# Optimization experiments

Measured on AMD Instinct MI355X. Metric: run time of the kernel, lower is better.

## Reference

```python
import math
import jax, jax.numpy as jnp
import numpy as np

B, T, C, H = 2, 2048, 1024, 16

def setup_inputs() -> dict:
    key = jax.random.key(0)
    k1, k2, k3 = jax.random.split(key, 3)
    x = jax.random.normal(k1, (B, T, C), dtype=jnp.float32)
    W_kqv = jax.random.normal(k2, (C, 3 * C), dtype=jnp.float32) * (1.0 / math.sqrt(C))
    W_proj = jax.random.normal(k3, (C, C), dtype=jnp.float32) * (1.0 / math.sqrt(C))
    b_proj = jnp.zeros((C,), dtype=jnp.float32)
    return {"x": x, "W_kqv": W_kqv, "W_proj": W_proj, "b_proj": b_proj}

def reference(x, W_kqv, W_proj, b_proj):
    Bx, Tx, Cx = x.shape
    hs = Cx // H  # head size
    q, k, v = jnp.split(x @ W_kqv, 3, axis=2)  # each (B,T,C)
    # (B,T,C) -> (B,H,T,hs)
    q = q.reshape(Bx, Tx, H, hs).transpose(0, 2, 1, 3)
    k = k.reshape(Bx, Tx, H, hs).transpose(0, 2, 1, 3)
    v = v.reshape(Bx, Tx, H, hs).transpose(0, 2, 1, 3)
    attn = jnp.einsum('bhqd,bhkd->bhqk', q, k) / math.sqrt(hs)  # (B,H,T,T)
    causal = jnp.tril(jnp.ones((Tx, Tx), dtype=bool))
    attn = jnp.where(causal, attn, -jnp.inf)
    attn = jax.nn.softmax(attn, axis=-1)
    y = jnp.einsum('bhqk,bhkd->bhqd', attn, v)  # (B,H,T,hs)
    y = y.transpose(0, 2, 1, 3).reshape(Bx, Tx, Cx)
    return y @ W_proj + b_proj
```

## Files before the change

### kernel.cpp

```cpp
#include <hip/hip_runtime.h>


typedef unsigned short u16;
typedef unsigned int u32;
typedef __bf16 bf16x8 __attribute__((ext_vector_type(8)));
typedef float f32x4 __attribute__((ext_vector_type(4)));
typedef u32 u32x4 __attribute__((ext_vector_type(4)));
typedef u16 u16x4 __attribute__((ext_vector_type(4)));

__device__ __forceinline__ u16 f2bf(float f) {
  u32 u = __float_as_uint(f);
  u32 r = u + 0x7FFFu + ((u >> 16) & 1u);
  return (u16)(r >> 16);
}

__device__ __forceinline__ bf16x8 ld_bf8(const u16* p) {
  union { u32x4 u; bf16x8 b; } x;
  x.u = *(const u32x4*)p;
  return x.b;
}

__device__ __forceinline__ void gld_lds16(const u16* g, u16* l) {
  __builtin_amdgcn_global_load_lds(
      (const __attribute__((address_space(1))) u32*)g,
      (__attribute__((address_space(3))) u32*)l, 16, 0, 0);
}

__global__ __launch_bounds__(256) void conv_x_kernel(const float* __restrict__ src,
                                                     u16* __restrict__ dst) {
  int idx = blockIdx.x * 256 + threadIdx.x;
  const float4* s4 = (const float4*)src;
  float4 a = s4[2 * idx], b = s4[2 * idx + 1];
  union { u16 h[8]; u32x4 v; } pk;
  pk.h[0] = f2bf(a.x); pk.h[1] = f2bf(a.y); pk.h[2] = f2bf(a.z); pk.h[3] = f2bf(a.w);
  pk.h[4] = f2bf(b.x); pk.h[5] = f2bf(b.y); pk.h[6] = f2bf(b.z); pk.h[7] = f2bf(b.w);
  *(u32x4*)&dst[(size_t)idx * 8] = pk.v;
}

__global__ __launch_bounds__(256) void convT_kernel(const float* __restrict__ src,
                                                    u16* __restrict__ dst, int R, int Cc) {
  __shared__ float ls[64][65];
  int r0 = blockIdx.x * 64, c0 = blockIdx.y * 64;
  int t = threadIdx.x;
  for (int u = t; u < 1024; u += 256) {
    int r = u >> 4, cs = (u & 15) << 2;
    float4 v = *(const float4*)&src[(size_t)(r0 + r) * Cc + (c0 + cs)];
    ls[r][cs] = v.x; ls[r][cs + 1] = v.y; ls[r][cs + 2] = v.z; ls[r][cs + 3] = v.w;
  }
  __syncthreads();
  for (int u = t; u < 1024; u += 256) {
    int n = u >> 4, ks = (u & 15) << 2;
    u16x4 o;
    o.x = f2bf(ls[ks][n]); o.y = f2bf(ls[ks + 1][n]);
    o.z = f2bf(ls[ks + 2][n]); o.w = f2bf(ls[ks + 3][n]);
    *(u16x4*)&dst[(size_t)(c0 + n) * R + (r0 + ks)] = o;
  }
}

__global__ __launch_bounds__(512) void qkv_gemm_kernel(
    const u16* __restrict__ A, const u16* __restrict__ Bt,
    u16* __restrict__ Qh, u16* __restrict__ Kh, u16* __restrict__ Vh, float qscale) {
  constexpr int K = 1024;
  __shared__ __align__(16) u16 As[128 * 32];
  __shared__ __align__(16) u16 Bs[128 * 32];
  int t = threadIdx.x;
  int wave = t >> 6, lane = t & 63, quad = lane >> 4, l16 = lane & 15;
  int wm = (wave >> 1) << 5, wn = (wave & 1) << 6;
  int m0 = blockIdx.x * 128, n0 = blockIdx.y * 128;
  f32x4 acc[2][4] = {};
  int u0 = t;
  int ra0 = u0 >> 2, ca0 = ((u0 & 3) ^ ((u0 >> 3) & 3)) << 3;
  int swq = (quad ^ ((l16 >> 1) & 3)) << 3;
  for (int k0 = 0; k0 < K; k0 += 32) {
    gld_lds16(&A[(size_t)(m0 + ra0) * K + k0 + ca0], &As[u0 * 8]);
    gld_lds16(&Bt[(size_t)(n0 + ra0) * K + k0 + ca0], &Bs[u0 * 8]);
    __syncthreads();
    bf16x8 af[2], bfr[4];
    for (int r = 0; r < 2; ++r) af[r] = ld_bf8(&As[(wm + r * 16 + l16) * 32 + swq]);
    for (int c = 0; c < 4; ++c) bfr[c] = ld_bf8(&Bs[(wn + c * 16 + l16) * 32 + swq]);
    for (int r = 0; r < 2; ++r)
      for (int c = 0; c < 4; ++c)
        acc[r][c] = __builtin_amdgcn_mfma_f32_16x16x32_bf16(af[r], bfr[c], acc[r][c], 0, 0, 0);
    __syncthreads();
  }
  for (int r = 0; r < 2; ++r) {
    int rowbase = m0 + wm + r * 16 + quad * 4;
    for (int c = 0; c < 4; ++c) {
      int col = n0 + wn + c * 16 + l16;
      int seg = col >> 10;
      int cc = col & 1023;
      int h = cc >> 6, d = cc & 63;
      for (int i = 0; i < 4; ++i) {
        int row = rowbase + i;
        int b = row >> 11, tt = row & 2047;
        size_t off = (((size_t)(b * 16 + h)) * 2048 + tt) * 64 + d;
        float v = acc[r][c][i];
        if (seg == 0)      Qh[off] = f2bf(v * qscale);
        else if (seg == 1) Kh[off] = f2bf(v);
        else               Vh[off] = f2bf(v);
      }
    }
  }
}

__global__ __launch_bounds__(256) void vT_kernel(const u16* __restrict__ Vh,
                                                 u16* __restrict__ Vt) {
  __shared__ __align__(16) u16 ls[64 * 72];
  int t = threadIdx.x;
  int t0 = blockIdx.x * 64, bh = blockIdx.y;
  const u16* in = Vh + ((size_t)bh * 2048 + t0) * 64;
  for (int u = t; u < 512; u += 256) {
    int row = u >> 3, col = (u & 7) << 3;
    *(u32x4*)&ls[row * 72 + col] = *(const u32x4*)&in[(size_t)row * 64 + col];
  }
  __syncthreads();
  for (int u = t; u < 512; u += 256) {
    int d = u >> 3, tc = (u & 7) << 3;
    union { u16 h[8]; u32x4 v; } pk;
    for (int j = 0; j < 8; ++j) pk.h[j] = ls[(tc + j) * 72 + d];
    *(u32x4*)&Vt[((size_t)bh * 64 + d) * 2048 + t0 + tc] = pk.v;
  }
}

__global__ __launch_bounds__(256) void proj_gemm_kernel(
    const u16* __restrict__ A, const u16* __restrict__ Bt,
    float* __restrict__ out, const float* __restrict__ bias) {
  constexpr int K = 1024;
  __shared__ __align__(16) u16 As[64 * 32];
  __shared__ __align__(16) u16 Bs[64 * 32];
  int t = threadIdx.x;
  int wave = t >> 6, lane = t & 63, quad = lane >> 4, l16 = lane & 15;
  int wm = (wave >> 1) << 5, wn = (wave & 1) << 5;
  int m0 = blockIdx.x * 64, n0 = blockIdx.y * 64;
  f32x4 acc[2][2] = {};
  int u0 = t;
  int ra0 = u0 >> 2, ca0 = ((u0 & 3) ^ ((u0 >> 3) & 3)) << 3;
  int swq = (quad ^ ((l16 >> 1) & 3)) << 3;
  for (int k0 = 0; k0 < K; k0 += 32) {
    gld_lds16(&A[(size_t)(m0 + ra0) * K + k0 + ca0], &As[u0 * 8]);
    gld_lds16(&Bt[(size_t)(n0 + ra0) * K + k0 + ca0], &Bs[u0 * 8]);
    __syncthreads();
    bf16x8 af[2], bfr[2];
    for (int r = 0; r < 2; ++r) af[r] = ld_bf8(&As[(wm + r * 16 + l16) * 32 + swq]);
    for (int c = 0; c < 2; ++c) bfr[c] = ld_bf8(&Bs[(wn + c * 16 + l16) * 32 + swq]);
    for (int r = 0; r < 2; ++r)
      for (int c = 0; c < 2; ++c)
        acc[r][c] = __builtin_amdgcn_mfma_f32_16x16x32_bf16(af[r], bfr[c], acc[r][c], 0, 0, 0);
    __syncthreads();
  }
  for (int r = 0; r < 2; ++r) {
    int rowbase = m0 + wm + r * 16 + quad * 4;
    for (int c = 0; c < 2; ++c) {
      int col = n0 + wn + c * 16 + l16;
      float bv = bias[col];
      for (int i = 0; i < 4; ++i)
        out[(size_t)(rowbase + i) * 1024 + col] = acc[r][c][i] + bv;
    }
  }
}

__global__ __launch_bounds__(256) void flash_kernel(
    const u16* __restrict__ Qh, const u16* __restrict__ Kh, const u16* __restrict__ Vt,
    u16* __restrict__ yb) {
  constexpr int LDK = 72;
  __shared__ __align__(16) u16 Ks[64 * LDK];
  __shared__ __align__(16) u16 Vs[64 * LDK];
  __shared__ __align__(16) u16 Ps[64 * LDK];
  int t = threadIdx.x, wave = t >> 6, lane = t & 63, quad = lane >> 4, l16 = lane & 15;
  int qtile = 31 - blockIdx.x;
  int bh = blockIdx.y;
  int q0 = qtile << 6;
  const u16* Qb = Qh + (size_t)bh * 2048 * 64;
  const u16* Kb = Kh + (size_t)bh * 2048 * 64;
  const u16* Vb = Vt + (size_t)bh * 64 * 2048;
  bf16x8 qa0, qa1;
  {
    int qrow = q0 + wave * 16 + l16;
    qa0 = ld_bf8(&Qb[(size_t)qrow * 64 + quad * 8]);
    qa1 = ld_bf8(&Qb[(size_t)qrow * 64 + 32 + quad * 8]);
  }
  bf16x8 onesf;
  {
    union { u16 h[8]; bf16x8 b; } o;
    u16 v = (l16 == 0) ? (u16)0x3F80 : (u16)0;
    for (int i = 0; i < 8; ++i) o.h[i] = v;
    onesf = o.b;
  }
  f32x4 oacc[4] = {};
  f32x4 lacc = {};
  int nkv = qtile + 1;
  int r1 = t >> 3, s1 = (t & 7) << 3, r2 = r1 + 32;
  u32x4 kreg0, kreg1, vreg0, vreg1;
  kreg0 = *(const u32x4*)&Kb[(size_t)r1 * 64 + s1];
  kreg1 = *(const u32x4*)&Kb[(size_t)r2 * 64 + s1];
  vreg0 = *(const u32x4*)&Vb[(size_t)r1 * 2048 + s1];
  vreg1 = *(const u32x4*)&Vb[(size_t)r2 * 2048 + s1];
  for (int j = 0; j < nkv; ++j) {
    __syncthreads();
    *(u32x4*)&Ks[r1 * LDK + s1] = kreg0;
    *(u32x4*)&Ks[r2 * LDK + s1] = kreg1;
    *(u32x4*)&Vs[r1 * LDK + s1] = vreg0;
    *(u32x4*)&Vs[r2 * LDK + s1] = vreg1;
    __syncthreads();
    if (j + 1 < nkv) {
      int kv0 = (j + 1) << 6;
      kreg0 = *(const u32x4*)&Kb[(size_t)(kv0 + r1) * 64 + s1];
      kreg1 = *(const u32x4*)&Kb[(size_t)(kv0 + r2) * 64 + s1];
      vreg0 = *(const u32x4*)&Vb[(size_t)r1 * 2048 + kv0 + s1];
      vreg1 = *(const u32x4*)&Vb[(size_t)r2 * 2048 + kv0 + s1];
    }
    f32x4 s[4];
    for (int c = 0; c < 4; ++c) {
      bf16x8 kb0 = ld_bf8(&Ks[(c * 16 + l16) * LDK + quad * 8]);
      bf16x8 kb1 = ld_bf8(&Ks[(c * 16 + l16) * LDK + 32 + quad * 8]);
      f32x4 z = {0.f, 0.f, 0.f, 0.f};
      z = __builtin_amdgcn_mfma_f32_16x16x32_bf16(qa0, kb0, z, 0, 0, 0);
      s[c] = __builtin_amdgcn_mfma_f32_16x16x32_bf16(qa1, kb1, z, 0, 0, 0);
    }
    bool diag = (j == nkv - 1);
    for (int c = 0; c < 4; ++c)
      for (int i = 0; i < 4; ++i) {
        float p = __builtin_amdgcn_exp2f(s[c][i]);
        if (diag && (c * 16 + l16 > wave * 16 + quad * 4 + i)) p = 0.f;
        Ps[(wave * 16 + quad * 4 + i) * LDK + c * 16 + l16] = f2bf(p);
      }
    bf16x8 pa0 = ld_bf8(&Ps[(wave * 16 + l16) * LDK + quad * 8]);
    bf16x8 pa1 = ld_bf8(&Ps[(wave * 16 + l16) * LDK + 32 + quad * 8]);
    lacc = __builtin_amdgcn_mfma_f32_16x16x32_bf16(pa0, onesf, lacc, 0, 0, 0);
    lacc = __builtin_amdgcn_mfma_f32_16x16x32_bf16(pa1, onesf, lacc, 0, 0, 0);
    for (int dt = 0; dt < 4; ++dt) {
      bf16x8 vb0 = ld_bf8(&Vs[(dt * 16 + l16) * LDK + quad * 8]);
      bf16x8 vb1 = ld_bf8(&Vs[(dt * 16 + l16) * LDK + 32 + quad * 8]);
      oacc[dt] = __builtin_amdgcn_mfma_f32_16x16x32_bf16(pa0, vb0, oacc[dt], 0, 0, 0);
      oacc[dt] = __builtin_amdgcn_mfma_f32_16x16x32_bf16(pa1, vb1, oacc[dt], 0, 0, 0);
    }
  }
  int b = bh >> 4, h = bh & 15;
  for (int i = 0; i < 4; ++i) {
    float l = __shfl(lacc[i], quad * 16);
    float inv = 1.0f / l;
    int qq = q0 + wave * 16 + quad * 4 + i;
    size_t rowoff = ((size_t)(b * 2048 + qq)) * 1024 + h * 64;
    for (int dt = 0; dt < 4; ++dt)
      yb[rowoff + dt * 16 + l16] = f2bf(oacc[dt][i] * inv);
  }
}

extern "C" void kernel_launch(void* const* d_in, const int* in_sizes, int n_in,
                              void* d_out, int out_size, void* d_ws, size_t ws_size,
                              hipStream_t stream) {
  const float* x     = (const float*)d_in[0];
  const float* Wkqv  = (const float*)d_in[1];
  const float* Wproj = (const float*)d_in[2];
  const float* bproj = (const float*)d_in[3];
  float* out = (float*)d_out;

  u16* ws     = (u16*)d_ws;
  u16* xb     = ws;
  u16* wkqvT  = xb + (size_t)4096 * 1024;
  u16* wprojT = wkqvT + (size_t)3072 * 1024;
  u16* Qh     = wprojT + (size_t)1024 * 1024;
  u16* Kh     = Qh + (size_t)32 * 2048 * 64;
  u16* Vt     = Kh + (size_t)32 * 2048 * 64;
  u16* yb     = Vt + (size_t)32 * 2048 * 64;
  u16* Vh     = yb;

  const float QSCALE = 0.18033688011112042f;

  conv_x_kernel<<<2048, 256, 0, stream>>>(x, xb);
  convT_kernel<<<dim3(16, 48), 256, 0, stream>>>(Wkqv, wkqvT, 1024, 3072);
  convT_kernel<<<dim3(16, 16), 256, 0, stream>>>(Wproj, wprojT, 1024, 1024);
  qkv_gemm_kernel<<<dim3(32, 24), 512, 0, stream>>>(xb, wkqvT, Qh, Kh, Vh, QSCALE);
  vT_kernel<<<dim3(32, 32), 256, 0, stream>>>(Vh, Vt);
  flash_kernel<<<dim3(32, 32), 256, 0, stream>>>(Qh, Kh, Vt, yb);
  proj_gemm_kernel<<<dim3(64, 16), 256, 0, stream>>>(yb, wprojT, out, bproj);
}
```

Before: 203.7 us.

## Split long causal query tiles across two blocks and merge with a combine kernel

The 13 longest causal query tiles per head are each split into two halves of their KV range, run as separate blocks. Each half writes unnormalized fp32 partial outputs and row sums to scratch, and a new combine kernel adds the halves and normalizes. The aim is to even out the causal work imbalance across blocks. The QK MFMA operands are also swapped, so each lane holds a query row; the row sum is then taken in registers with two shuffles instead of an extra ones-MFMA, and P is stored to LDS as 4-wide vectors. The cost is an extra launch plus fp32 scratch traffic, with the scratch aliased over workspace regions that are no longer needed.

```diff
diff --git a/kernel.cpp b/kernel.cpp
--- a/kernel.cpp
+++ b/kernel.cpp
@@ -161,14 +161,23 @@
 
 __global__ __launch_bounds__(256) void flash_kernel(
     const u16* __restrict__ Qh, const u16* __restrict__ Kh, const u16* __restrict__ Vt,
-    u16* __restrict__ yb) {
+    u16* __restrict__ yb, float* __restrict__ Opart) {
   constexpr int LDK = 72;
   __shared__ __align__(16) u16 Ks[64 * LDK];
   __shared__ __align__(16) u16 Vs[64 * LDK];
   __shared__ __align__(16) u16 Ps[64 * LDK];
   int t = threadIdx.x, wave = t >> 6, lane = t & 63, quad = lane >> 4, l16 = lane & 15;
-  int qtile = 31 - blockIdx.x;
-  int bh = blockIdx.y;
+  int jx = blockIdx.x, bh = blockIdx.y;
+  int qtile, kvs, kve, sidx = 0, half = 0;
+  bool partial;
+  if (jx < 19) {
+    qtile = 18 - jx; kvs = 0; kve = qtile + 1; partial = false;
+  } else {
+    sidx = (jx - 19) >> 1; half = (jx - 19) & 1;
+    qtile = 31 - sidx;
+    int nkv = qtile + 1, mid = nkv >> 1;
+    kvs = half ? mid : 0; kve = half ? nkv : mid; partial = true;
+  }
   int q0 = qtile << 6;
   const u16* Qb = Qh + (size_t)bh * 2048 * 64;
   const u16* Kb = Kh + (size_t)bh * 2048 * 64;
@@ -179,55 +188,54 @@
     qa0 = ld_bf8(&Qb[(size_t)qrow * 64 + quad * 8]);
     qa1 = ld_bf8(&Qb[(size_t)qrow * 64 + 32 + quad * 8]);
   }
-  bf16x8 onesf;
-  {
-    union { u16 h[8]; bf16x8 b; } o;
-    u16 v = (l16 == 0) ? (u16)0x3F80 : (u16)0;
-    for (int i = 0; i < 8; ++i) o.h[i] = v;
-    onesf = o.b;
-  }
   f32x4 oacc[4] = {};
-  f32x4 lacc = {};
-  int nkv = qtile + 1;
+  float lsum = 0.f;
   int r1 = t >> 3, s1 = (t & 7) << 3, r2 = r1 + 32;
   u32x4 kreg0, kreg1, vreg0, vreg1;
-  kreg0 = *(const u32x4*)&Kb[(size_t)r1 * 64 + s1];
-  kreg1 = *(const u32x4*)&Kb[(size_t)r2 * 64 + s1];
-  vreg0 = *(const u32x4*)&Vb[(size_t)r1 * 2048 + s1];
-  vreg1 = *(const u32x4*)&Vb[(size_t)r2 * 2048 + s1];
-  for (int j = 0; j < nkv; ++j) {
+  {
+    int kv0 = kvs << 6;
+    kreg0 = *(const u32x4*)&Kb[(size_t)(kv0 + r1) * 64 + s1];
+    kreg1 = *(const u32x4*)&Kb[(size_t)(kv0 + r2) * 64 + s1];
+    vreg0 = *(const u32x4*)&Vb[(size_t)r1 * 2048 + kv0 + s1];
+    vreg1 = *(const u32x4*)&Vb[(size_t)r2 * 2048 + kv0 + s1];
+  }
+  for (int j = kvs; j < kve; ++j) {
+    int kv0 = j << 6;
     __syncthreads();
     *(u32x4*)&Ks[r1 * LDK + s1] = kreg0;
     *(u32x4*)&Ks[r2 * LDK + s1] = kreg1;
     *(u32x4*)&Vs[r1 * LDK + s1] = vreg0;
     *(u32x4*)&Vs[r2 * LDK + s1] = vreg1;
     __syncthreads();
-    if (j + 1 < nkv) {
-      int kv0 = (j + 1) << 6;
-      kreg0 = *(const u32x4*)&Kb[(size_t)(kv0 + r1) * 64 + s1];
-      kreg1 = *(const u32x4*)&Kb[(size_t)(kv0 + r2) * 64 + s1];
-      vreg0 = *(const u32x4*)&Vb[(size_t)r1 * 2048 + kv0 + s1];
-      vreg1 = *(const u32x4*)&Vb[(size_t)r2 * 2048 + kv0 + s1];
+    if (j + 1 < kve) {
+      int kn = (j + 1) << 6;
+      kreg0 = *(const u32x4*)&Kb[(size_t)(kn + r1) * 64 + s1];
+      kreg1 = *(const u32x4*)&Kb[(size_t)(kn + r2) * 64 + s1];
+      vreg0 = *(const u32x4*)&Vb[(size_t)r1 * 2048 + kn + s1];
+      vreg1 = *(const u32x4*)&Vb[(size_t)r2 * 2048 + kn + s1];
     }
     f32x4 s[4];
     for (int c = 0; c < 4; ++c) {
       bf16x8 kb0 = ld_bf8(&Ks[(c * 16 + l16) * LDK + quad * 8]);
       bf16x8 kb1 = ld_bf8(&Ks[(c * 16 + l16) * LDK + 32 + quad * 8]);
       f32x4 z = {0.f, 0.f, 0.f, 0.f};
-      z = __builtin_amdgcn_mfma_f32_16x16x32_bf16(qa0, kb0, z, 0, 0, 0);
-      s[c] = __builtin_amdgcn_mfma_f32_16x16x32_bf16(qa1, kb1, z, 0, 0, 0);
-    }
-    bool diag = (j == nkv - 1);
-    for (int c = 0; c < 4; ++c)
+      z = __builtin_amdgcn_mfma_f32_16x16x32_bf16(kb0, qa0, z, 0, 0, 0);
+      s[c] = __builtin_amdgcn_mfma_f32_16x16x32_bf16(kb1, qa1, s[c] = z, 0, 0, 0);
+    }
+    bool diag = (j == qtile);
+    int qg = q0 + wave * 16 + l16;
+    for (int c = 0; c < 4; ++c) {
+      union { u16 h[4]; u16x4 v; } pk;
       for (int i = 0; i < 4; ++i) {
         float p = __builtin_amdgcn_exp2f(s[c][i]);
-        if (diag && (c * 16 + l16 > wave * 16 + quad * 4 + i)) p = 0.f;
-        Ps[(wave * 16 + quad * 4 + i) * LDK + c * 16 + l16] = f2bf(p);
+        if (diag && (kv0 + c * 16 + quad * 4 + i > qg)) p = 0.f;
+        lsum += p;
+        pk.h[i] = f2bf(p);
       }
+      *(u16x4*)&Ps[(wave * 16 + l16) * LDK + c * 16 + quad * 4] = pk.v;
+    }
     bf16x8 pa0 = ld_bf8(&Ps[(wave * 16 + l16) * LDK + quad * 8]);
     bf16x8 pa1 = ld_bf8(&Ps[(wave * 16 + l16) * LDK + 32 + quad * 8]);
-    lacc = __builtin_amdgcn_mfma_f32_16x16x32_bf16(pa0, onesf, lacc, 0, 0, 0);
-    lacc = __builtin_amdgcn_mfma_f32_16x16x32_bf16(pa1, onesf, lacc, 0, 0, 0);
     for (int dt = 0; dt < 4; ++dt) {
       bf16x8 vb0 = ld_bf8(&Vs[(dt * 16 + l16) * LDK + quad * 8]);
       bf16x8 vb1 = ld_bf8(&Vs[(dt * 16 + l16) * LDK + 32 + quad * 8]);
@@ -235,15 +243,41 @@
       oacc[dt] = __builtin_amdgcn_mfma_f32_16x16x32_bf16(pa1, vb1, oacc[dt], 0, 0, 0);
     }
   }
+  lsum += __shfl_xor(lsum, 16);
+  lsum += __shfl_xor(lsum, 32);
+  if (partial) {
+    float* Op = Opart + ((size_t)(bh * 13 + sidx) * 2 + half) * 4160;
+    for (int dt = 0; dt < 4; ++dt)
+      for (int i = 0; i < 4; ++i)
+        Op[(wave * 16 + quad * 4 + i) * 64 + dt * 16 + l16] = oacc[dt][i];
+    if (quad == 0) Op[4096 + wave * 16 + l16] = lsum;
+  } else {
+    int b = bh >> 4, h = bh & 15;
+    for (int i = 0; i < 4; ++i) {
+      float inv = 1.0f / __shfl(lsum, quad * 4 + i);
+      int qq = q0 + wave * 16 + quad * 4 + i;
+      size_t rowoff = ((size_t)(b * 2048 + qq)) * 1024 + h * 64;
+      for (int dt = 0; dt < 4; ++dt)
+        yb[rowoff + dt * 16 + l16] = f2bf(oacc[dt][i] * inv);
+    }
+  }
+}
+
+__global__ __launch_bounds__(256) void combine_kernel(const float* __restrict__ Opart,
+                                                      u16* __restrict__ yb) {
+  int sidx = blockIdx.x, bh = blockIdx.y, t = threadIdx.x;
+  int qtile = 31 - sidx;
+  const float* A = Opart + (size_t)(bh * 13 + sidx) * 2 * 4160;
+  const float* Bp = A + 4160;
+  int q = t >> 2, d0 = (t & 3) << 4;
+  float inv = 1.0f / (A[4096 + q] + Bp[4096 + q]);
   int b = bh >> 4, h = bh & 15;
-  for (int i = 0; i < 4; ++i) {
-    float l = __shfl(lacc[i], quad * 16);
-    float inv = 1.0f / l;
-    int qq = q0 + wave * 16 + quad * 4 + i;
-    size_t rowoff = ((size_t)(b * 2048 + qq)) * 1024 + h * 64;
-    for (int dt = 0; dt < 4; ++dt)
-      yb[rowoff + dt * 16 + l16] = f2bf(oacc[dt][i] * inv);
-  }
+  size_t off = ((size_t)(b * 2048 + (qtile << 6) + q)) * 1024 + h * 64 + d0;
+  union { u16 h[16]; u32x4 v[2]; } pk;
+  for (int k = 0; k < 16; ++k)
+    pk.h[k] = f2bf((A[q * 64 + d0 + k] + Bp[q * 64 + d0 + k]) * inv);
+  *(u32x4*)&yb[off] = pk.v[0];
+  *(u32x4*)&yb[off + 8] = pk.v[1];
 }
 
 extern "C" void kernel_launch(void* const* d_in, const int* in_sizes, int n_in,
@@ -264,6 +298,7 @@
   u16* Vt     = Kh + (size_t)32 * 2048 * 64;
   u16* yb     = Vt + (size_t)32 * 2048 * 64;
   u16* Vh     = yb;
+  float* Opart = (float*)ws;
 
   const float QSCALE = 0.18033688011112042f;
 
@@ -272,6 +307,7 @@
   convT_kernel<<<dim3(16, 16), 256, 0, stream>>>(Wproj, wprojT, 1024, 1024);
   qkv_gemm_kernel<<<dim3(32, 24), 512, 0, stream>>>(xb, wkqvT, Qh, Kh, Vh, QSCALE);
   vT_kernel<<<dim3(32, 32), 256, 0, stream>>>(Vh, Vt);
-  flash_kernel<<<dim3(32, 32), 256, 0, stream>>>(Qh, Kh, Vt, yb);
+  flash_kernel<<<dim3(45, 32), 256, 0, stream>>>(Qh, Kh, Vt, yb, Opart);
+  combine_kernel<<<dim3(13, 32), 256, 0, stream>>>(Opart, yb);
   proj_gemm_kernel<<<dim3(64, 16), 256, 0, stream>>>(yb, wprojT, out, bproj);
 }
```

Result: faster. 191.4 us (-6.0%).

## Split long causal attention tiles across blocks and retile QKV and projection GEMMs

Applied to the files above, without the earlier changes.

The flash kernel moves to 128-row query tiles and maps 22 jobs per head through constant tables. The six longest query tiles are each split into two KV halves, which write fp32 partial outputs and row sums to workspace; a new combine kernel merges them, the aim being to balance causal work across blocks. Row sums are now taken with VALU adds and shuffles instead of an extra MFMA against a ones vector, and the K/V/P shared-memory layouts use an XOR-style swizzle in place of padding. Both GEMMs are retiled: QKV runs 4x4 MFMA tiles per wave with 256 threads, and projection uses 128x128 blocks with 512 threads. The costs are an extra launch, partial-result traffic through workspace that aliases the earlier buffers, and higher register pressure.

```diff
diff --git a/kernel.cpp b/kernel.cpp
--- a/kernel.cpp
+++ b/kernel.cpp
@@ -7,6 +7,9 @@
 typedef float f32x4 __attribute__((ext_vector_type(4)));
 typedef u32 u32x4 __attribute__((ext_vector_type(4)));
 typedef u16 u16x4 __attribute__((ext_vector_type(4)));
+
+__constant__ signed char JM[22] = {9,8,7,15,15,14,14,6,13,13,12,12,5,11,11,10,10,4,3,2,1,0};
+__constant__ signed char JH[22] = {0,0,0,1, 2, 1, 2, 0,1, 2, 1, 2, 0,1, 2, 1, 2, 0,0,0,0,0};
 
 __device__ __forceinline__ u16 f2bf(float f) {
   u32 u = __float_as_uint(f);
@@ -57,7 +60,7 @@
   }
 }
 
-__global__ __launch_bounds__(512) void qkv_gemm_kernel(
+__global__ __launch_bounds__(256) void qkv_gemm_kernel(
     const u16* __restrict__ A, const u16* __restrict__ Bt,
     u16* __restrict__ Qh, u16* __restrict__ Kh, u16* __restrict__ Vh, float qscale) {
   constexpr int K = 1024;
@@ -65,25 +68,28 @@
   __shared__ __align__(16) u16 Bs[128 * 32];
   int t = threadIdx.x;
   int wave = t >> 6, lane = t & 63, quad = lane >> 4, l16 = lane & 15;
-  int wm = (wave >> 1) << 5, wn = (wave & 1) << 6;
+  int wm = (wave >> 1) << 6, wn = (wave & 1) << 6;
   int m0 = blockIdx.x * 128, n0 = blockIdx.y * 128;
-  f32x4 acc[2][4] = {};
-  int u0 = t;
+  f32x4 acc[4][4] = {};
+  int u0 = t, u1 = t + 256;
   int ra0 = u0 >> 2, ca0 = ((u0 & 3) ^ ((u0 >> 3) & 3)) << 3;
+  int ra1 = u1 >> 2, ca1 = ((u1 & 3) ^ ((u1 >> 3) & 3)) << 3;
   int swq = (quad ^ ((l16 >> 1) & 3)) << 3;
   for (int k0 = 0; k0 < K; k0 += 32) {
     gld_lds16(&A[(size_t)(m0 + ra0) * K + k0 + ca0], &As[u0 * 8]);
+    gld_lds16(&A[(size_t)(m0 + ra1) * K + k0 + ca1], &As[u1 * 8]);
     gld_lds16(&Bt[(size_t)(n0 + ra0) * K + k0 + ca0], &Bs[u0 * 8]);
-    __syncthreads();
-    bf16x8 af[2], bfr[4];
-    for (int r = 0; r < 2; ++r) af[r] = ld_bf8(&As[(wm + r * 16 + l16) * 32 + swq]);
+    gld_lds16(&Bt[(size_t)(n0 + ra1) * K + k0 + ca1], &Bs[u1 * 8]);
+    __syncthreads();
+    bf16x8 af[4], bfr[4];
+    for (int r = 0; r < 4; ++r) af[r] = ld_bf8(&As[(wm + r * 16 + l16) * 32 + swq]);
     for (int c = 0; c < 4; ++c) bfr[c] = ld_bf8(&Bs[(wn + c * 16 + l16) * 32 + swq]);
-    for (int r = 0; r < 2; ++r)
+    for (int r = 0; r < 4; ++r)
       for (int c = 0; c < 4; ++c)
         acc[r][c] = __builtin_amdgcn_mfma_f32_16x16x32_bf16(af[r], bfr[c], acc[r][c], 0, 0, 0);
     __syncthreads();
   }
-  for (int r = 0; r < 2; ++r) {
+  for (int r = 0; r < 4; ++r) {
     int rowbase = m0 + wm + r * 16 + quad * 4;
     for (int c = 0; c < 4; ++c) {
       int col = n0 + wn + c * 16 + l16;
@@ -122,17 +128,17 @@
   }
 }
 
-__global__ __launch_bounds__(256) void proj_gemm_kernel(
+__global__ __launch_bounds__(512) void proj_gemm_kernel(
     const u16* __restrict__ A, const u16* __restrict__ Bt,
     float* __restrict__ out, const float* __restrict__ bias) {
   constexpr int K = 1024;
-  __shared__ __align__(16) u16 As[64 * 32];
-  __shared__ __align__(16) u16 Bs[64 * 32];
+  __shared__ __align__(16) u16 As[128 * 32];
+  __shared__ __align__(16) u16 Bs[128 * 32];
   int t = threadIdx.x;
   int wave = t >> 6, lane = t & 63, quad = lane >> 4, l16 = lane & 15;
-  int wm = (wave >> 1) << 5, wn = (wave & 1) << 5;
-  int m0 = blockIdx.x * 64, n0 = blockIdx.y * 64;
-  f32x4 acc[2][2] = {};
+  int wm = (wave >> 2) << 6, wn = (wave & 3) << 5;
+  int m0 = blockIdx.x * 128, n0 = blockIdx.y * 128;
+  f32x4 acc[4][2] = {};
   int u0 = t;
   int ra0 = u0 >> 2, ca0 = ((u0 & 3) ^ ((u0 >> 3) & 3)) << 3;
   int swq = (quad ^ ((l16 >> 1) & 3)) << 3;
@@ -140,15 +146,15 @@
     gld_lds16(&A[(size_t)(m0 + ra0) * K + k0 + ca0], &As[u0 * 8]);
     gld_lds16(&Bt[(size_t)(n0 + ra0) * K + k0 + ca0], &Bs[u0 * 8]);
     __syncthreads();
-    bf16x8 af[2], bfr[2];
-    for (int r = 0; r < 2; ++r) af[r] = ld_bf8(&As[(wm + r * 16 + l16) * 32 + swq]);
+    bf16x8 af[4], bfr[2];
+    for (int r = 0; r < 4; ++r) af[r] = ld_bf8(&As[(wm + r * 16 + l16) * 32 + swq]);
     for (int c = 0; c < 2; ++c) bfr[c] = ld_bf8(&Bs[(wn + c * 16 + l16) * 32 + swq]);
-    for (int r = 0; r < 2; ++r)
+    for (int r = 0; r < 4; ++r)
       for (int c = 0; c < 2; ++c)
         acc[r][c] = __builtin_amdgcn_mfma_f32_16x16x32_bf16(af[r], bfr[c], acc[r][c], 0, 0, 0);
     __syncthreads();
   }
-  for (int r = 0; r < 2; ++r) {
+  for (int r = 0; r < 4; ++r) {
     int rowbase = m0 + wm + r * 16 + quad * 4;
     for (int c = 0; c < 2; ++c) {
       int col = n0 + wn + c * 16 + l16;
@@ -161,88 +167,135 @@
 
 __global__ __launch_bounds__(256) void flash_kernel(
     const u16* __restrict__ Qh, const u16* __restrict__ Kh, const u16* __restrict__ Vt,
-    u16* __restrict__ yb) {
-  constexpr int LDK = 72;
-  __shared__ __align__(16) u16 Ks[64 * LDK];
-  __shared__ __align__(16) u16 Vs[64 * LDK];
-  __shared__ __align__(16) u16 Ps[64 * LDK];
+    u16* __restrict__ yb, float* __restrict__ Opart) {
+  __shared__ __align__(16) u16 Ks[64 * 64];
+  __shared__ __align__(16) u16 Vs[64 * 64];
+  __shared__ __align__(16) u16 Ps[128 * 64];
   int t = threadIdx.x, wave = t >> 6, lane = t & 63, quad = lane >> 4, l16 = lane & 15;
-  int qtile = 31 - blockIdx.x;
-  int bh = blockIdx.y;
-  int q0 = qtile << 6;
+  int jx = blockIdx.x, bh = blockIdx.y;
+  int m = JM[jx], jh = JH[jx];
+  int kvs = (jh == 2) ? (m + 1) : 0;
+  int kve = (jh == 1) ? (m + 1) : (2 * m + 2);
+  bool partial = jh != 0;
+  int q0 = m << 7;
   const u16* Qb = Qh + (size_t)bh * 2048 * 64;
   const u16* Kb = Kh + (size_t)bh * 2048 * 64;
   const u16* Vb = Vt + (size_t)bh * 64 * 2048;
-  bf16x8 qa0, qa1;
+  bf16x8 qa[2][2];
+  for (int s = 0; s < 2; ++s) {
+    int qrow = q0 + wave * 32 + s * 16 + l16;
+    qa[s][0] = ld_bf8(&Qb[(size_t)qrow * 64 + quad * 8]);
+    qa[s][1] = ld_bf8(&Qb[(size_t)qrow * 64 + 32 + quad * 8]);
+  }
+  f32x4 oacc[2][4] = {};
+  float ls0 = 0.f, ls1 = 0.f;
+  int ua = t, ub = t + 256;
+  int ra = ua >> 3, cba = ua & 7, rb = ub >> 3, cbb = ub & 7;
+  int lka = ra * 64 + ((cba + ra) & 7) * 8;
+  int lkb = rb * 64 + ((cbb + rb) & 7) * 8;
+  u32x4 kreg0, kreg1, vreg0, vreg1;
   {
-    int qrow = q0 + wave * 16 + l16;
-    qa0 = ld_bf8(&Qb[(size_t)qrow * 64 + quad * 8]);
-    qa1 = ld_bf8(&Qb[(size_t)qrow * 64 + 32 + quad * 8]);
-  }
-  bf16x8 onesf;
-  {
-    union { u16 h[8]; bf16x8 b; } o;
-    u16 v = (l16 == 0) ? (u16)0x3F80 : (u16)0;
-    for (int i = 0; i < 8; ++i) o.h[i] = v;
-    onesf = o.b;
-  }
-  f32x4 oacc[4] = {};
-  f32x4 lacc = {};
-  int nkv = qtile + 1;
-  int r1 = t >> 3, s1 = (t & 7) << 3, r2 = r1 + 32;
-  u32x4 kreg0, kreg1, vreg0, vreg1;
-  kreg0 = *(const u32x4*)&Kb[(size_t)r1 * 64 + s1];
-  kreg1 = *(const u32x4*)&Kb[(size_t)r2 * 64 + s1];
-  vreg0 = *(const u32x4*)&Vb[(size_t)r1 * 2048 + s1];
-  vreg1 = *(const u32x4*)&Vb[(size_t)r2 * 2048 + s1];
-  for (int j = 0; j < nkv; ++j) {
-    __syncthreads();
-    *(u32x4*)&Ks[r1 * LDK + s1] = kreg0;
-    *(u32x4*)&Ks[r2 * LDK + s1] = kreg1;
-    *(u32x4*)&Vs[r1 * LDK + s1] = vreg0;
-    *(u32x4*)&Vs[r2 * LDK + s1] = vreg1;
-    __syncthreads();
-    if (j + 1 < nkv) {
-      int kv0 = (j + 1) << 6;
-      kreg0 = *(const u32x4*)&Kb[(size_t)(kv0 + r1) * 64 + s1];
-      kreg1 = *(const u32x4*)&Kb[(size_t)(kv0 + r2) * 64 + s1];
-      vreg0 = *(const u32x4*)&Vb[(size_t)r1 * 2048 + kv0 + s1];
-      vreg1 = *(const u32x4*)&Vb[(size_t)r2 * 2048 + kv0 + s1];
-    }
-    f32x4 s[4];
+    int kv0 = kvs << 6;
+    kreg0 = *(const u32x4*)&Kb[(size_t)(kv0 + ra) * 64 + cba * 8];
+    kreg1 = *(const u32x4*)&Kb[(size_t)(kv0 + rb) * 64 + cbb * 8];
+    vreg0 = *(const u32x4*)&Vb[(size_t)ra * 2048 + kv0 + cba * 8];
+    vreg1 = *(const u32x4*)&Vb[(size_t)rb * 2048 + kv0 + cbb * 8];
+  }
+  for (int j = kvs; j < kve; ++j) {
+    int kv0 = j << 6;
+    __syncthreads();
+    *(u32x4*)&Ks[lka] = kreg0;
+    *(u32x4*)&Ks[lkb] = kreg1;
+    *(u32x4*)&Vs[lka] = vreg0;
+    *(u32x4*)&Vs[lkb] = vreg1;
+    __syncthreads();
+    if (j + 1 < kve) {
+      int kn = (j + 1) << 6;
+      kreg0 = *(const u32x4*)&Kb[(size_t)(kn + ra) * 64 + cba * 8];
+      kreg1 = *(const u32x4*)&Kb[(size_t)(kn + rb) * 64 + cbb * 8];
+      vreg0 = *(const u32x4*)&Vb[(size_t)ra * 2048 + kn + cba * 8];
+      vreg1 = *(const u32x4*)&Vb[(size_t)rb * 2048 + kn + cbb * 8];
+    }
+    bool maskit = (j >= 2 * m);
     for (int c = 0; c < 4; ++c) {
-      bf16x8 kb0 = ld_bf8(&Ks[(c * 16 + l16) * LDK + quad * 8]);
-      bf16x8 kb1 = ld_bf8(&Ks[(c * 16 + l16) * LDK + 32 + quad * 8]);
-      f32x4 z = {0.f, 0.f, 0.f, 0.f};
-      z = __builtin_amdgcn_mfma_f32_16x16x32_bf16(qa0, kb0, z, 0, 0, 0);
-      s[c] = __builtin_amdgcn_mfma_f32_16x16x32_bf16(qa1, kb1, z, 0, 0, 0);
-    }
-    bool diag = (j == nkv - 1);
-    for (int c = 0; c < 4; ++c)
+      int krow = c * 16 + l16;
+      bf16x8 kb0 = ld_bf8(&Ks[krow * 64 + ((quad + krow) & 7) * 8]);
+      bf16x8 kb1 = ld_bf8(&Ks[krow * 64 + ((quad + 4 + krow) & 7) * 8]);
+      for (int s = 0; s < 2; ++s) {
+        f32x4 z = {0.f, 0.f, 0.f, 0.f};
+        z = __builtin_amdgcn_mfma_f32_16x16x32_bf16(kb0, qa[s][0], z, 0, 0, 0);
+        z = __builtin_amdgcn_mfma_f32_16x16x32_bf16(kb1, qa[s][1], z, 0, 0, 0);
+        int prow = wave * 32 + s * 16 + l16;
+        union { u16 hh[4]; u16x4 v; } pk;
+        float lsadd = 0.f;
+        for (int i = 0; i < 4; ++i) {
+          float p = __builtin_amdgcn_exp2f(z[i]);
+          if (maskit && (kv0 + c * 16 + quad * 4 + i > q0 + prow)) p = 0.f;
+          lsadd += p;
+          pk.hh[i] = f2bf(p);
+        }
+        if (s) ls1 += lsadd; else ls0 += lsadd;
+        *(u16x4*)&Ps[prow * 64 + ((2 * c + (quad >> 1) + prow) & 7) * 8 + (quad & 1) * 4] = pk.v;
+      }
+    }
+    bf16x8 pa[2][2];
+    for (int s = 0; s < 2; ++s) {
+      int prow = wave * 32 + s * 16 + l16;
+      pa[s][0] = ld_bf8(&Ps[prow * 64 + ((quad + prow) & 7) * 8]);
+      pa[s][1] = ld_bf8(&Ps[prow * 64 + ((quad + 4 + prow) & 7) * 8]);
+    }
+    for (int dt = 0; dt < 4; ++dt) {
+      int vrow = dt * 16 + l16;
+      bf16x8 vb0 = ld_bf8(&Vs[vrow * 64 + ((quad + vrow) & 7) * 8]);
+      bf16x8 vb1 = ld_bf8(&Vs[vrow * 64 + ((quad + 4 + vrow) & 7) * 8]);
+      for (int s = 0; s < 2; ++s) {
+        oacc[s][dt] = __builtin_amdgcn_mfma_f32_16x16x32_bf16(pa[s][0], vb0, oacc[s][dt], 0, 0, 0);
+        oacc[s][dt] = __builtin_amdgcn_mfma_f32_16x16x32_bf16(pa[s][1], vb1, oacc[s][dt], 0, 0, 0);
+      }
+    }
+  }
+  ls0 += __shfl_xor(ls0, 16); ls0 += __shfl_xor(ls0, 32);
+  ls1 += __shfl_xor(ls1, 16); ls1 += __shfl_xor(ls1, 32);
+  if (partial) {
+    float* Op = Opart + ((size_t)(bh * 6 + (m - 10)) * 2 + (jh - 1)) * 8320;
+    for (int s = 0; s < 2; ++s)
+      for (int dt = 0; dt < 4; ++dt)
+        for (int i = 0; i < 4; ++i)
+          Op[(wave * 32 + s * 16 + quad * 4 + i) * 64 + dt * 16 + l16] = oacc[s][dt][i];
+    if (quad == 0) {
+      Op[8192 + wave * 32 + l16] = ls0;
+      Op[8192 + wave * 32 + 16 + l16] = ls1;
+    }
+  } else {
+    int b = bh >> 4, hh = bh & 15;
+    for (int s = 0; s < 2; ++s) {
+      float lss = s ? ls1 : ls0;
       for (int i = 0; i < 4; ++i) {
-        float p = __builtin_amdgcn_exp2f(s[c][i]);
-        if (diag && (c * 16 + l16 > wave * 16 + quad * 4 + i)) p = 0.f;
-        Ps[(wave * 16 + quad * 4 + i) * LDK + c * 16 + l16] = f2bf(p);
+        float inv = 1.0f / __shfl(lss, quad * 4 + i);
+        int qq = q0 + wave * 32 + s * 16 + quad * 4 + i;
+        size_t rowoff = ((size_t)(b * 2048 + qq)) * 1024 + hh * 64;
+        for (int dt = 0; dt < 4; ++dt)
+          yb[rowoff + dt * 16 + l16] = f2bf(oacc[s][dt][i] * inv);
       }
-    bf16x8 pa0 = ld_bf8(&Ps[(wave * 16 + l16) * LDK + quad * 8]);
-    bf16x8 pa1 = ld_bf8(&Ps[(wave * 16 + l16) * LDK + 32 + quad * 8]);
-    lacc = __builtin_amdgcn_mfma_f32_16x16x32_bf16(pa0, onesf, lacc, 0, 0, 0);
-    lacc = __builtin_amdgcn_mfma_f32_16x16x32_bf16(pa1, onesf, lacc, 0, 0, 0);
-    for (int dt = 0; dt < 4; ++dt) {
-      bf16x8 vb0 = ld_bf8(&Vs[(dt * 16 + l16) * LDK + quad * 8]);
-      bf16x8 vb1 = ld_bf8(&Vs[(dt * 16 + l16) * LDK + 32 + quad * 8]);
-      oacc[dt] = __builtin_amdgcn_mfma_f32_16x16x32_bf16(pa0, vb0, oacc[dt], 0, 0, 0);
-      oacc[dt] = __builtin_amdgcn_mfma_f32_16x16x32_bf16(pa1, vb1, oacc[dt], 0, 0, 0);
-    }
-  }
+    }
+  }
+}
+
+__global__ __launch_bounds__(256) void combine_kernel(const float* __restrict__ Opart,
+                                                      u16* __restrict__ yb) {
+  int sx = blockIdx.x, bh = blockIdx.y, t = threadIdx.x;
+  int m = 10 + sx;
+  const float* A = Opart + (size_t)(bh * 6 + sx) * 2 * 8320;
+  const float* Bp = A + 8320;
+  int q = t >> 1, d0 = (t & 1) << 5;
+  float inv = 1.0f / (A[8192 + q] + Bp[8192 + q]);
   int b = bh >> 4, h = bh & 15;
-  for (int i = 0; i < 4; ++i) {
-    float l = __shfl(lacc[i], quad * 16);
-    float inv = 1.0f / l;
-    int qq = q0 + wave * 16 + quad * 4 + i;
-    size_t rowoff = ((size_t)(b * 2048 + qq)) * 1024 + h * 64;
-    for (int dt = 0; dt < 4; ++dt)
-      yb[rowoff + dt * 16 + l16] = f2bf(oacc[dt][i] * inv);
+  size_t off = ((size_t)(b * 2048 + (m << 7) + q)) * 1024 + h * 64 + d0;
+  for (int k0 = 0; k0 < 32; k0 += 8) {
+    union { u16 hh[8]; u32x4 v; } pk;
+    for (int k = 0; k < 8; ++k)
+      pk.hh[k] = f2bf((A[q * 64 + d0 + k0 + k] + Bp[q * 64 + d0 + k0 + k]) * inv);
+    *(u32x4*)&yb[off + k0] = pk.v;
   }
 }
 
@@ -264,14 +317,16 @@
   u16* Vt     = Kh + (size_t)32 * 2048 * 64;
   u16* yb     = Vt + (size_t)32 * 2048 * 64;
   u16* Vh     = yb;
+  float* Opart = (float*)ws;
 
   const float QSCALE = 0.18033688011112042f;
 
   conv_x_kernel<<<2048, 256, 0, stream>>>(x, xb);
   convT_kernel<<<dim3(16, 48), 256, 0, stream>>>(Wkqv, wkqvT, 1024, 3072);
   convT_kernel<<<dim3(16, 16), 256, 0, stream>>>(Wproj, wprojT, 1024, 1024);
-  qkv_gemm_kernel<<<dim3(32, 24), 512, 0, stream>>>(xb, wkqvT, Qh, Kh, Vh, QSCALE);
+  qkv_gemm_kernel<<<dim3(32, 24), 256, 0, stream>>>(xb, wkqvT, Qh, Kh, Vh, QSCALE);
   vT_kernel<<<dim3(32, 32), 256, 0, stream>>>(Vh, Vt);
-  flash_kernel<<<dim3(32, 32), 256, 0, stream>>>(Qh, Kh, Vt, yb);
-  proj_gemm_kernel<<<dim3(64, 16), 256, 0, stream>>>(yb, wprojT, out, bproj);
-}
+  flash_kernel<<<dim3(22, 32), 256, 0, stream>>>(Qh, Kh, Vt, yb, Opart);
+  combine_kernel<<<dim3(6, 32), 256, 0, stream>>>(Opart, yb);
+  proj_gemm_kernel<<<dim3(32, 8), 512, 0, stream>>>(yb, wprojT, out, bproj);
+}
```

New measurement: 198.7 us. 1.03x faster.
